# Optimization experiments

Hardware: AMD Instinct MI355X
Metric: run time of the kernel (lower is better)

## Reference

```python
import jax, jax.numpy as jnp
import numpy as np

NUM_HEADS = 16
DIM = 1024
HEAD_DIM = DIM // NUM_HEADS
SCALE = HEAD_DIM ** -0.5


def setup_inputs() -> dict:
    key = jax.random.key(0)
    ks = jax.random.split(key, 6)
    b, n = 2, 1024
    x = jax.random.normal(ks[0], (b, n, DIM), dtype=jnp.float32)
    Wq = jax.random.normal(ks[1], (DIM, DIM), dtype=jnp.float32) * 0.02
    bq = jnp.zeros((DIM,), dtype=jnp.float32)
    Wkv = jax.random.normal(ks[2], (2 * DIM, DIM), dtype=jnp.float32) * 0.02
    bkv = jnp.zeros((2 * DIM,), dtype=jnp.float32)
    Wp = jax.random.normal(ks[3], (DIM, DIM), dtype=jnp.float32) * 0.02
    bp = jnp.zeros((DIM,), dtype=jnp.float32)
    return {"x": x, "Wq": Wq, "bq": bq, "Wkv": Wkv, "bkv": bkv, "Wp": Wp, "bp": bp}


def reference(x, Wq, bq, Wkv, bkv, Wp, bp):
    b, n, c = x.shape
    h, dh = NUM_HEADS, HEAD_DIM
    # self-attention: y = x
    q = (x @ Wq.T + bq).reshape(b, n, h, dh)              # bnhd
    kv = (x @ Wkv.T + bkv).reshape(b, n, 2, h, dh)
    k, v = kv[:, :, 0], kv[:, :, 1]                       # bmhd each
    attn = jnp.einsum('bnhd,bmhd->bnmh', q, k) * SCALE    # bnmh scores
    attn = jax.nn.softmax(attn, axis=2)                   # softmax over m
    out = jnp.einsum('bnmh,bmhd->bnhd', attn, v).reshape(b, n, c)
    out = out @ Wp.T + bp
    return (out, attn)
```

## Files before the change

kernel.cpp:

```cpp
#include <hip/hip_runtime.h>
#include <hip/hip_bf16.h>
#include <stdint.h>


#define NB   2
#define SEQ  1024
#define CDIM 1024
#define NH   16
#define HD   64
#define ROWS (NB*SEQ)
#define ATT_SCALE 0.125f

typedef __attribute__((ext_vector_type(8))) short bf16x8;
typedef __attribute__((ext_vector_type(4))) float f32x4;

#define MFMA16(a,b,c) __builtin_amdgcn_mfma_f32_16x16x32_bf16((a),(b),(c),0,0,0)

static __device__ __forceinline__ unsigned short f2bf(float f) {
  uint32_t x = __builtin_bit_cast(uint32_t, f);
  return (unsigned short)((x + 0x7fffu + ((x >> 16) & 1u)) >> 16);
}
static __device__ __forceinline__ float bf2f(unsigned short u) {
  uint32_t x = ((uint32_t)u) << 16;
  return __builtin_bit_cast(float, x);
}

static __device__ __forceinline__ void gl_lds16(const unsigned short* g,
                                                unsigned short* l) {
  __builtin_amdgcn_global_load_lds(
      (const __attribute__((address_space(1))) unsigned int*)g,
      (__attribute__((address_space(3))) unsigned int*)l,
      16, 0, 0);
}

__global__ __launch_bounds__(256) void k_convert(
    const float* __restrict__ x, const float* __restrict__ Wq,
    const float* __restrict__ Wkv, const float* __restrict__ Wp,
    unsigned short* __restrict__ Xhi, unsigned short* __restrict__ Xlo,
    unsigned short* __restrict__ Whi, unsigned short* __restrict__ Wlo)
{
  const int NX = ROWS * CDIM;
  const int NW = 4096 * CDIM;
  int i = blockIdx.x * 256 + threadIdx.x;
  if (i < NX) {
    float f = x[i];
    unsigned short h = f2bf(f);
    Xhi[i] = h; Xlo[i] = f2bf(f - bf2f(h));
  } else if (i < NX + NW) {
    int w = i - NX;
    int j = w >> 10, c = w & 1023;
    float f = (j < 1024) ? Wq[(size_t)j*1024 + c]
            : (j < 3072) ? Wkv[(size_t)(j-1024)*1024 + c]
                         : Wp[(size_t)(j-3072)*1024 + c];
    unsigned short h = f2bf(f);
    Whi[w] = h; Wlo[w] = f2bf(f - bf2f(h));
  }
}

struct EpiQKV {
  const float* bq; const float* bkv;
  unsigned short *Qhi, *Qlo, *Khi, *Klo, *Vthi, *Vtlo;
  __device__ __forceinline__ void operator()(int m, int n, float v) const {
    if (n < 1024) {
      v = (v + bq[n]) * ATT_SCALE;
      unsigned short h = f2bf(v);
      size_t o = (size_t)m*1024 + n;
      Qhi[o] = h; Qlo[o] = f2bf(v - bf2f(h));
    } else if (n < 2048) {
      v += bkv[n - 1024];
      size_t o = (size_t)m*1024 + (n - 1024);
      unsigned short h = f2bf(v);
      Khi[o] = h; Klo[o] = f2bf(v - bf2f(h));
    } else {
      v += bkv[n - 1024];
      int c = n - 2048;
      int hh = c >> 6, d = c & 63;
      int b = m >> 10, mm = m & 1023;
      size_t o = ((size_t)((b*NH + hh)*HD + d))*SEQ + mm;
      unsigned short h = f2bf(v);
      Vthi[o] = h; Vtlo[o] = f2bf(v - bf2f(h));
    }
  }
};
struct EpiOut {
  const float* bp; float* out;
  __device__ __forceinline__ void operator()(int m, int n, float v) const {
    out[(size_t)m*1024 + n] = v + bp[n];
  }
};

template <int BM, int BN, class Epi>
__device__ __forceinline__ void gemm_core(
    const unsigned short* __restrict__ Ahi, const unsigned short* __restrict__ Alo, int lda,
    const unsigned short* __restrict__ Bhi, const unsigned short* __restrict__ Blo, int ldb,
    int K, const Epi& epi)
{
  constexpr int FM = BM/32, FN = BN/32;
  constexpr int CA = BM/16, CB = BN/16;
  constexpr int TOT = 2*(CA+CB);
  __shared__ unsigned short sAh[BM*32], sAl[BM*32], sBh[BN*32], sBl[BN*32];
  const int tid  = threadIdx.x;
  const int lane = tid & 63, wave = tid >> 6;
  const int wm = wave & 1, wn = wave >> 1;
  const int bn = blockIdx.x * BN, bm = blockIdx.y * BM;
  const int r = lane & 15, q = lane >> 4;
  const int crow = lane >> 2, ccol = (lane & 3) * 8;

  f32x4 acc[FM][FN];
  #pragma unroll
  for (int i = 0; i < FM; i++)
    #pragma unroll
    for (int j = 0; j < FN; j++) {
      acc[i][j][0]=0.f; acc[i][j][1]=0.f; acc[i][j][2]=0.f; acc[i][j][3]=0.f;
    }

  for (int k0 = 0; k0 < K; k0 += 32) {
    #pragma unroll
    for (int t = 0; t < TOT/4; t++) {
      int c = wave + t*4;
      const unsigned short* gb; unsigned short* sb; int rr, grow, ld;
      if (c < CA)            { gb=Ahi; sb=sAh; rr=c;         grow=bm; ld=lda; }
      else if (c < 2*CA)     { gb=Alo; sb=sAl; rr=c-CA;      grow=bm; ld=lda; }
      else if (c < 2*CA+CB)  { gb=Bhi; sb=sBh; rr=c-2*CA;    grow=bn; ld=ldb; }
      else                   { gb=Blo; sb=sBl; rr=c-2*CA-CB; grow=bn; ld=ldb; }
      int row = rr*16 + crow;
      gl_lds16(gb + (size_t)(grow + row)*ld + k0 + ccol, sb + rr*512);
    }
    __syncthreads();
    bf16x8 ah[FM], al[FM], bh[FN], bl[FN];
    #pragma unroll
    for (int i = 0; i < FM; i++) {
      int oa = (wm*(BM/2) + i*16 + r)*32 + q*8;
      ah[i] = *(const bf16x8*)(sAh + oa);
      al[i] = *(const bf16x8*)(sAl + oa);
    }
    #pragma unroll
    for (int j = 0; j < FN; j++) {
      int ob = (wn*(BN/2) + j*16 + r)*32 + q*8;
      bh[j] = *(const bf16x8*)(sBh + ob);
      bl[j] = *(const bf16x8*)(sBl + ob);
    }
    #pragma unroll
    for (int i = 0; i < FM; i++)
      #pragma unroll
      for (int j = 0; j < FN; j++) {
        acc[i][j] = MFMA16(ah[i], bh[j], acc[i][j]);
        acc[i][j] = MFMA16(ah[i], bl[j], acc[i][j]);
        acc[i][j] = MFMA16(al[i], bh[j], acc[i][j]);
      }
    __syncthreads();
  }
  #pragma unroll
  for (int i = 0; i < FM; i++)
    #pragma unroll
    for (int j = 0; j < FN; j++)
      #pragma unroll
      for (int t = 0; t < 4; t++)
        epi(bm + wm*(BM/2) + i*16 + q*4 + t, bn + wn*(BN/2) + j*16 + r, acc[i][j][t]);
}

__global__ __launch_bounds__(256) void k_gemm_qkv(
    const unsigned short* Xhi, const unsigned short* Xlo,
    const unsigned short* Whi, const unsigned short* Wlo,
    const float* bq, const float* bkv,
    unsigned short* Qhi, unsigned short* Qlo,
    unsigned short* Khi, unsigned short* Klo,
    unsigned short* Vthi, unsigned short* Vtlo)
{
  EpiQKV e{bq, bkv, Qhi, Qlo, Khi, Klo, Vthi, Vtlo};
  gemm_core<128,128>(Xhi, Xlo, CDIM, Whi, Wlo, CDIM, CDIM, e);
}

__global__ __launch_bounds__(256) void k_gemm_out(
    const unsigned short* OAhi, const unsigned short* OAlo,
    const unsigned short* Wphi, const unsigned short* Wplo,
    const float* bp, float* out)
{
  EpiOut e{bp, out};
  gemm_core<64,64>(OAhi, OAlo, CDIM, Wphi, Wplo, CDIM, CDIM, e);
}

__global__ __launch_bounds__(512, 4) void k_logits_softmax(
    const unsigned short* __restrict__ Qhi, const unsigned short* __restrict__ Qlo,
    const unsigned short* __restrict__ Khi, const unsigned short* __restrict__ Klo,
    unsigned short* __restrict__ P)
{
  const int nt = blockIdx.x, h = blockIdx.y, b = blockIdx.z;
  const int n0 = nt*32;
  const int col0 = h*HD;
  __shared__ unsigned short sQ[2*32*64];
  __shared__ unsigned short sK[2][2*128*64];
  __shared__ float redm[8][32], reds[8][32];
  __shared__ float gm_s[32], sc_s[32];
  const int tid = threadIdx.x, lane = tid & 63, wave = tid >> 6;
  const int r = lane & 15, q = lane >> 4;
  const int drow = lane >> 3, dseg = (lane & 7) ^ drow;
  const int sw = r & 7;
  const size_t qrow0 = (size_t)b*SEQ + n0;
  const size_t krow0 = (size_t)b*SEQ;

  auto stageK = [&](int c, int buf) {
    unsigned short* dst = sK[buf];
    #pragma unroll
    for (int u = 0; u < 4; u++) {
      int cc = wave*4 + u;
      int p = cc >> 4, t = cc & 15;
      const unsigned short* g = p ? Klo : Khi;
      gl_lds16(g + (krow0 + (size_t)c*128 + t*8 + drow)*CDIM + col0 + dseg*8,
               dst + p*8192 + t*512);
    }
  };

  {
    int p = wave >> 2, t = wave & 3;
    const unsigned short* g = p ? Qlo : Qhi;
    gl_lds16(g + (qrow0 + t*8 + drow)*CDIM + col0 + dseg*8,
             sQ + p*2048 + t*512);
    stageK(0, 0);
  }
  __syncthreads();

  bf16x8 qh[2][2], ql[2][2];
  #pragma unroll
  for (int nf = 0; nf < 2; nf++)
    #pragma unroll
    for (int ks = 0; ks < 2; ks++) {
      int phys = (nf*16 + r)*64 + (((ks*4 + q) ^ sw))*8;
      qh[nf][ks] = *(const bf16x8*)(sQ + phys);
      ql[nf][ks] = *(const bf16x8*)(sQ + 2048 + phys);
    }

  const int mb = wave*16;

  float mx[2] = {-1e30f, -1e30f}, sm[2] = {0.f, 0.f};
  for (int c = 0; c < 8; c++) {
    if (c < 7) stageK(c+1, (c+1)&1);
    const unsigned short* cur = sK[c&1];
    bf16x8 kh[2], kl[2];
    #pragma unroll
    for (int ks = 0; ks < 2; ks++) {
      int phys = (mb + r)*64 + (((ks*4 + q) ^ sw))*8;
      kh[ks] = *(const bf16x8*)(cur + phys);
      kl[ks] = *(const bf16x8*)(cur + 8192 + phys);
    }
    #pragma unroll
    for (int nf = 0; nf < 2; nf++) {
      f32x4 acc; acc[0]=0.f; acc[1]=0.f; acc[2]=0.f; acc[3]=0.f;
      #pragma unroll
      for (int ks = 0; ks < 2; ks++) {
        acc = MFMA16(kh[ks], qh[nf][ks], acc);
        acc = MFMA16(kl[ks], qh[nf][ks], acc);
        acc = MFMA16(kh[ks], ql[nf][ks], acc);
      }
      float vmax = fmaxf(fmaxf(acc[0], acc[1]), fmaxf(acc[2], acc[3]));
      float mnew = fmaxf(mx[nf], vmax);
      sm[nf] = sm[nf]*__expf(mx[nf]-mnew)
             + __expf(acc[0]-mnew) + __expf(acc[1]-mnew)
             + __expf(acc[2]-mnew) + __expf(acc[3]-mnew);
      mx[nf] = mnew;
    }
    __syncthreads();
  }

  #pragma unroll
  for (int nf = 0; nf < 2; nf++) {
    #pragma unroll
    for (int off = 16; off <= 32; off <<= 1) {
      float mo = __shfl_xor(mx[nf], off);
      float so = __shfl_xor(sm[nf], off);
      float mn = fmaxf(mx[nf], mo);
      sm[nf] = sm[nf]*__expf(mx[nf]-mn) + so*__expf(mo-mn);
      mx[nf] = mn;
    }
  }
  if (q < 2) { redm[wave][q*16 + r] = mx[q]; reds[wave][q*16 + r] = sm[q]; }
  stageK(0, 0);
  __syncthreads();
  if (tid < 32) {
    float m2 = redm[0][tid], s2 = reds[0][tid];
    #pragma unroll
    for (int w2 = 1; w2 < 8; w2++) {
      float mo = redm[w2][tid], so = reds[w2][tid];
      float mn = fmaxf(m2, mo);
      s2 = s2*__expf(m2-mn) + so*__expf(mo-mn);
      m2 = mn;
    }
    gm_s[tid] = m2; sc_s[tid] = 65535.0f / s2;
  }
  __syncthreads();
  const float gm[2] = {gm_s[r], gm_s[16 + r]};
  const float sc[2] = {sc_s[r], sc_s[16 + r]};

  const size_t pbase = ((size_t)(b*NH + h)*SEQ + n0)*SEQ;
  for (int c = 0; c < 8; c++) {
    if (c < 7) stageK(c+1, (c+1)&1);
    const unsigned short* cur = sK[c&1];
    bf16x8 kh[2], kl[2];
    #pragma unroll
    for (int ks = 0; ks < 2; ks++) {
      int phys = (mb + r)*64 + (((ks*4 + q) ^ sw))*8;
      kh[ks] = *(const bf16x8*)(cur + phys);
      kl[ks] = *(const bf16x8*)(cur + 8192 + phys);
    }
    #pragma unroll
    for (int nf = 0; nf < 2; nf++) {
      f32x4 acc; acc[0]=0.f; acc[1]=0.f; acc[2]=0.f; acc[3]=0.f;
      #pragma unroll
      for (int ks = 0; ks < 2; ks++) {
        acc = MFMA16(kh[ks], qh[nf][ks], acc);
        acc = MFMA16(kl[ks], qh[nf][ks], acc);
        acc = MFMA16(kh[ks], ql[nf][ks], acc);
      }
      unsigned int u0 = (unsigned)(__expf(acc[0]-gm[nf])*sc[nf] + 0.5f)
                      | ((unsigned)(__expf(acc[1]-gm[nf])*sc[nf] + 0.5f) << 16);
      unsigned int u1 = (unsigned)(__expf(acc[2]-gm[nf])*sc[nf] + 0.5f)
                      | ((unsigned)(__expf(acc[3]-gm[nf])*sc[nf] + 0.5f) << 16);
      *(uint2*)(P + pbase + (size_t)(nf*16 + r)*SEQ + c*128 + mb + q*4) =
          make_uint2(u0, u1);
    }
    __syncthreads();
  }
}

__global__ __launch_bounds__(256) void k_attn_write(
    const unsigned short* __restrict__ P, float* __restrict__ attn)
{
  int T = blockIdx.x*256 + threadIdx.x;
  int b = T >> 20, rem = T & 1048575;
  int n = rem >> 10, m = rem & 1023;
  const size_t pb = ((size_t)(b*NH)*SEQ + n)*SEQ + m;
  float v[16];
  #pragma unroll
  for (int h = 0; h < 16; h++)
    v[h] = (float)P[pb + (size_t)h*SEQ*SEQ] * (1.0f/65535.0f);
  size_t ob = ((size_t)(b*SEQ + n)*SEQ + m)*16;
  #pragma unroll
  for (int g = 0; g < 4; g++)
    *(float4*)(attn + ob + g*4) = make_float4(v[g*4], v[g*4+1], v[g*4+2], v[g*4+3]);
}

__global__ __launch_bounds__(256) void k_pv(
    const unsigned short* __restrict__ P,
    const unsigned short* __restrict__ Vthi, const unsigned short* __restrict__ Vtlo,
    unsigned short* __restrict__ OAhi, unsigned short* __restrict__ OAlo)
{
  int nt = blockIdx.x, h = blockIdx.y, b = blockIdx.z;
  int n0 = nt * 64;
  __shared__ unsigned short sPa[64*32], sPb[64*32], sVh[64*32], sVl[64*32];
  const int tid = threadIdx.x, lane = tid & 63, wave = tid >> 6;
  const int wm = wave & 1, wn = wave >> 1;
  const int r = lane & 15, q = lane >> 4;
  const int crow = lane >> 2, ccol = (lane & 3) * 8;
  const size_t pbase = ((size_t)(b*NH + h))*SEQ*SEQ;
  const size_t vbase = ((size_t)(b*NH + h))*HD*SEQ;

  f32x4 acc[2][2];
  #pragma unroll
  for (int i = 0; i < 2; i++)
    #pragma unroll
    for (int j = 0; j < 2; j++) {
      acc[i][j][0]=0.f; acc[i][j][1]=0.f; acc[i][j][2]=0.f; acc[i][j][3]=0.f;
    }

  for (int k0 = 0; k0 < SEQ; k0 += 32) {
    #pragma unroll
    for (int t = 0; t < 2; t++) {
      int c = wave + t*4;
      const unsigned short* gb = (c < 4) ? Vthi : Vtlo;
      unsigned short* sb = (c < 4) ? (unsigned short*)sVh : (unsigned short*)sVl;
      int rr = c & 3;
      int row = rr*16 + crow;
      gl_lds16(gb + vbase + (size_t)row*SEQ + k0 + ccol, sb + rr*512);
    }
    {
      int row = tid >> 2, ch = (tid & 3) * 8;
      uint4 v = *(const uint4*)(P + pbase + (size_t)(n0 + row)*SEQ + k0 + ch);
      unsigned int wds[4] = {v.x, v.y, v.z, v.w};
      unsigned int pa[4], pb4[4];
      #pragma unroll
      for (int e = 0; e < 4; e++) {
        unsigned int lo16 = wds[e] & 0xFFFFu;
        unsigned int hi16 = wds[e] >> 16;
        unsigned int a0 = __builtin_bit_cast(uint32_t, (float)(lo16 & 0xFF00u)) >> 16;
        unsigned int b0 = __builtin_bit_cast(uint32_t, (float)(lo16 & 0x00FFu)) >> 16;
        unsigned int a1 = __builtin_bit_cast(uint32_t, (float)(hi16 & 0xFF00u)) >> 16;
        unsigned int b1 = __builtin_bit_cast(uint32_t, (float)(hi16 & 0x00FFu)) >> 16;
        pa[e]  = a0 | (a1 << 16);
        pb4[e] = b0 | (b1 << 16);
      }
      *(uint4*)(sPa + row*32 + ch) = make_uint4(pa[0],pa[1],pa[2],pa[3]);
      *(uint4*)(sPb + row*32 + ch) = make_uint4(pb4[0],pb4[1],pb4[2],pb4[3]);
    }
    __syncthreads();
    bf16x8 pa[2], pb2[2], vh[2], vl[2];
    #pragma unroll
    for (int i = 0; i < 2; i++) {
      int off = (wm*32 + i*16 + r)*32 + q*8;
      pa[i]  = *(const bf16x8*)(sPa + off);
      pb2[i] = *(const bf16x8*)(sPb + off);
    }
    #pragma unroll
    for (int j = 0; j < 2; j++) {
      int off = (wn*32 + j*16 + r)*32 + q*8;
      vh[j] = *(const bf16x8*)(sVh + off);
      vl[j] = *(const bf16x8*)(sVl + off);
    }
    #pragma unroll
    for (int i = 0; i < 2; i++)
      #pragma unroll
      for (int j = 0; j < 2; j++) {
        acc[i][j] = MFMA16(pa[i],  vh[j], acc[i][j]);
        acc[i][j] = MFMA16(pb2[i], vh[j], acc[i][j]);
        acc[i][j] = MFMA16(pa[i],  vl[j], acc[i][j]);
      }
    __syncthreads();
  }
  #pragma unroll
  for (int i = 0; i < 2; i++)
    #pragma unroll
    for (int t = 0; t < 4; t++) {
      int nn = n0 + wm*32 + i*16 + q*4 + t;
      #pragma unroll
      for (int j = 0; j < 2; j++) {
        int d = wn*32 + j*16 + r;
        float val = acc[i][j][t] * (1.0f/65535.0f);
        size_t o = (size_t)(b*SEQ + nn)*CDIM + h*HD + d;
        unsigned short hb = f2bf(val);
        OAhi[o] = hb; OAlo[o] = f2bf(val - bf2f(hb));
      }
    }
}

extern "C" void kernel_launch(void* const* d_in, const int* in_sizes, int n_in,
                              void* d_out, int out_size, void* d_ws, size_t ws_size,
                              hipStream_t stream)
{
  const float* x   = (const float*)d_in[0];
  const float* Wq  = (const float*)d_in[1];
  const float* bq  = (const float*)d_in[2];
  const float* Wkv = (const float*)d_in[3];
  const float* bkv = (const float*)d_in[4];
  const float* Wp  = (const float*)d_in[5];
  const float* bp  = (const float*)d_in[6];

  float* out  = (float*)d_out;
  float* attn = out + (size_t)ROWS*CDIM;

  char* w = (char*)d_ws;
  unsigned short* Xhi  = (unsigned short*)w; w += (size_t)ROWS*CDIM*2;
  unsigned short* Xlo  = (unsigned short*)w; w += (size_t)ROWS*CDIM*2;
  unsigned short* Whi  = (unsigned short*)w; w += (size_t)4096*CDIM*2;
  unsigned short* Wlo  = (unsigned short*)w; w += (size_t)4096*CDIM*2;
  unsigned short* Qhi  = (unsigned short*)w; w += (size_t)ROWS*CDIM*2;
  unsigned short* Qlo  = (unsigned short*)w; w += (size_t)ROWS*CDIM*2;
  unsigned short* Khi  = (unsigned short*)w; w += (size_t)ROWS*CDIM*2;
  unsigned short* Klo  = (unsigned short*)w; w += (size_t)ROWS*CDIM*2;
  unsigned short* Vthi = (unsigned short*)w; w += (size_t)NB*NH*HD*SEQ*2;
  unsigned short* Vtlo = (unsigned short*)w; w += (size_t)NB*NH*HD*SEQ*2;
  unsigned short* OAhi = (unsigned short*)w; w += (size_t)ROWS*CDIM*2;
  unsigned short* OAlo = (unsigned short*)w; w += (size_t)ROWS*CDIM*2;
  unsigned short* P    = (unsigned short*)w; w += (size_t)NB*NH*SEQ*SEQ*2;

  k_convert<<<dim3((ROWS*CDIM + 4096*CDIM)/256), 256, 0, stream>>>(
      x, Wq, Wkv, Wp, Xhi, Xlo, Whi, Wlo);

  k_gemm_qkv<<<dim3(3072/128, 2048/128), 256, 0, stream>>>(
      Xhi, Xlo, Whi, Wlo, bq, bkv, Qhi, Qlo, Khi, Klo, Vthi, Vtlo);

  k_logits_softmax<<<dim3(SEQ/32, NH, NB), 512, 0, stream>>>(
      Qhi, Qlo, Khi, Klo, P);

  k_pv<<<dim3(SEQ/64, NH, NB), 256, 0, stream>>>(P, Vthi, Vtlo, OAhi, OAlo);

  k_gemm_out<<<dim3(1024/64, 2048/64), 256, 0, stream>>>(
      OAhi, OAlo, Whi + (size_t)3072*CDIM, Wlo + (size_t)3072*CDIM, bp, out);

  k_attn_write<<<dim3((NB*SEQ*SEQ)/256), 256, 0, stream>>>(P, attn);
}
```

Baseline: 394.5 us.

## Single-pass softmax with per-chunk rescale factors; retile output projection GEMM

The logits kernel now computes QK^T only once. Each 128-column chunk is quantized against the running row max, and a per-chunk correction factor (exp(m_c - m_final)/sum) is stored in a small table. The PV and attn_write kernels apply these factors, PV by folding them into its accumulator every 128 columns. This removes the second QK^T pass and its K re-staging, at the cost of an extra sync per chunk and some precision loss when early chunks are quantized against a smaller max. Separately, the output GEMM moves to 128x64 tiles with 8 waves, which halves its grid.

```diff
diff --git a/kernel.cpp b/kernel.cpp
--- a/kernel.cpp
+++ b/kernel.cpp
@@ -89,19 +89,20 @@
   }
 };
 
-template <int BM, int BN, class Epi>
+template <int BM, int BN, int WM, int WN, class Epi>
 __device__ __forceinline__ void gemm_core(
     const unsigned short* __restrict__ Ahi, const unsigned short* __restrict__ Alo, int lda,
     const unsigned short* __restrict__ Bhi, const unsigned short* __restrict__ Blo, int ldb,
     int K, const Epi& epi)
 {
-  constexpr int FM = BM/32, FN = BN/32;
+  constexpr int WAVES = WM*WN;
+  constexpr int FM = BM/(WM*16), FN = BN/(WN*16);
   constexpr int CA = BM/16, CB = BN/16;
   constexpr int TOT = 2*(CA+CB);
   __shared__ unsigned short sAh[BM*32], sAl[BM*32], sBh[BN*32], sBl[BN*32];
   const int tid  = threadIdx.x;
   const int lane = tid & 63, wave = tid >> 6;
-  const int wm = wave & 1, wn = wave >> 1;
+  const int wm = wave % WM, wn = wave / WM;
   const int bn = blockIdx.x * BN, bm = blockIdx.y * BM;
   const int r = lane & 15, q = lane >> 4;
   const int crow = lane >> 2, ccol = (lane & 3) * 8;
@@ -116,8 +117,8 @@
 
   for (int k0 = 0; k0 < K; k0 += 32) {
     #pragma unroll
-    for (int t = 0; t < TOT/4; t++) {
-      int c = wave + t*4;
+    for (int t = 0; t < TOT/WAVES; t++) {
+      int c = wave + t*WAVES;
       const unsigned short* gb; unsigned short* sb; int rr, grow, ld;
       if (c < CA)            { gb=Ahi; sb=sAh; rr=c;         grow=bm; ld=lda; }
       else if (c < 2*CA)     { gb=Alo; sb=sAl; rr=c-CA;      grow=bm; ld=lda; }
@@ -130,13 +131,13 @@
     bf16x8 ah[FM], al[FM], bh[FN], bl[FN];
     #pragma unroll
     for (int i = 0; i < FM; i++) {
-      int oa = (wm*(BM/2) + i*16 + r)*32 + q*8;
+      int oa = (wm*(BM/WM) + i*16 + r)*32 + q*8;
       ah[i] = *(const bf16x8*)(sAh + oa);
       al[i] = *(const bf16x8*)(sAl + oa);
     }
     #pragma unroll
     for (int j = 0; j < FN; j++) {
-      int ob = (wn*(BN/2) + j*16 + r)*32 + q*8;
+      int ob = (wn*(BN/WN) + j*16 + r)*32 + q*8;
       bh[j] = *(const bf16x8*)(sBh + ob);
       bl[j] = *(const bf16x8*)(sBl + ob);
     }
@@ -156,7 +157,7 @@
     for (int j = 0; j < FN; j++)
       #pragma unroll
       for (int t = 0; t < 4; t++)
-        epi(bm + wm*(BM/2) + i*16 + q*4 + t, bn + wn*(BN/2) + j*16 + r, acc[i][j][t]);
+        epi(bm + wm*(BM/WM) + i*16 + q*4 + t, bn + wn*(BN/WN) + j*16 + r, acc[i][j][t]);
 }
 
 __global__ __launch_bounds__(256) void k_gemm_qkv(
@@ -168,30 +169,31 @@
     unsigned short* Vthi, unsigned short* Vtlo)
 {
   EpiQKV e{bq, bkv, Qhi, Qlo, Khi, Klo, Vthi, Vtlo};
-  gemm_core<128,128>(Xhi, Xlo, CDIM, Whi, Wlo, CDIM, CDIM, e);
-}
-
-__global__ __launch_bounds__(256) void k_gemm_out(
+  gemm_core<128,128,2,2>(Xhi, Xlo, CDIM, Whi, Wlo, CDIM, CDIM, e);
+}
+
+__global__ __launch_bounds__(512) void k_gemm_out(
     const unsigned short* OAhi, const unsigned short* OAlo,
     const unsigned short* Wphi, const unsigned short* Wplo,
     const float* bp, float* out)
 {
   EpiOut e{bp, out};
-  gemm_core<64,64>(OAhi, OAlo, CDIM, Wphi, Wplo, CDIM, CDIM, e);
+  gemm_core<128,64,4,2>(OAhi, OAlo, CDIM, Wphi, Wplo, CDIM, CDIM, e);
 }
 
 __global__ __launch_bounds__(512, 4) void k_logits_softmax(
     const unsigned short* __restrict__ Qhi, const unsigned short* __restrict__ Qlo,
     const unsigned short* __restrict__ Khi, const unsigned short* __restrict__ Klo,
-    unsigned short* __restrict__ P)
+    unsigned short* __restrict__ P, float* __restrict__ F)
 {
   const int nt = blockIdx.x, h = blockIdx.y, b = blockIdx.z;
   const int n0 = nt*32;
   const int col0 = h*HD;
   __shared__ unsigned short sQ[2*32*64];
   __shared__ unsigned short sK[2][2*128*64];
-  __shared__ float redm[8][32], reds[8][32];
-  __shared__ float gm_s[32], sc_s[32];
+  __shared__ float redm[2][8][32];
+  __shared__ float reds[8][32];
+  __shared__ float musd[32][8];
   const int tid = threadIdx.x, lane = tid & 63, wave = tid >> 6;
   const int r = lane & 15, q = lane >> 4;
   const int drow = lane >> 3, dseg = (lane & 7) ^ drow;
@@ -231,8 +233,9 @@
     }
 
   const int mb = wave*16;
-
-  float mx[2] = {-1e30f, -1e30f}, sm[2] = {0.f, 0.f};
+  float m_run[2] = {-1e30f, -1e30f}, s_run[2] = {0.f, 0.f};
+  const size_t pbase = ((size_t)(b*NH + h)*SEQ + n0)*SEQ;
+
   for (int c = 0; c < 8; c++) {
     if (c < 7) stageK(c+1, (c+1)&1);
     const unsigned short* cur = sK[c&1];
@@ -243,96 +246,82 @@
       kh[ks] = *(const bf16x8*)(cur + phys);
       kl[ks] = *(const bf16x8*)(cur + 8192 + phys);
     }
+    f32x4 acc[2];
     #pragma unroll
     for (int nf = 0; nf < 2; nf++) {
-      f32x4 acc; acc[0]=0.f; acc[1]=0.f; acc[2]=0.f; acc[3]=0.f;
+      acc[nf][0]=0.f; acc[nf][1]=0.f; acc[nf][2]=0.f; acc[nf][3]=0.f;
       #pragma unroll
       for (int ks = 0; ks < 2; ks++) {
-        acc = MFMA16(kh[ks], qh[nf][ks], acc);
-        acc = MFMA16(kl[ks], qh[nf][ks], acc);
-        acc = MFMA16(kh[ks], ql[nf][ks], acc);
+        acc[nf] = MFMA16(kh[ks], qh[nf][ks], acc[nf]);
+        acc[nf] = MFMA16(kl[ks], qh[nf][ks], acc[nf]);
+        acc[nf] = MFMA16(kh[ks], ql[nf][ks], acc[nf]);
       }
-      float vmax = fmaxf(fmaxf(acc[0], acc[1]), fmaxf(acc[2], acc[3]));
-      float mnew = fmaxf(mx[nf], vmax);
-      sm[nf] = sm[nf]*__expf(mx[nf]-mnew)
-             + __expf(acc[0]-mnew) + __expf(acc[1]-mnew)
-             + __expf(acc[2]-mnew) + __expf(acc[3]-mnew);
-      mx[nf] = mnew;
-    }
+    }
+    float wmax[2];
+    #pragma unroll
+    for (int nf = 0; nf < 2; nf++) {
+      float v = fmaxf(fmaxf(acc[nf][0], acc[nf][1]), fmaxf(acc[nf][2], acc[nf][3]));
+      v = fmaxf(v, __shfl_xor(v, 16));
+      v = fmaxf(v, __shfl_xor(v, 32));
+      wmax[nf] = v;
+    }
+    if (q == 0) { redm[c&1][wave][r] = wmax[0]; redm[c&1][wave][16+r] = wmax[1]; }
     __syncthreads();
+    #pragma unroll
+    for (int nf = 0; nf < 2; nf++) {
+      int row = nf*16 + r;
+      float mc = redm[c&1][0][row];
+      #pragma unroll
+      for (int w2 = 1; w2 < 8; w2++) mc = fmaxf(mc, redm[c&1][w2][row]);
+      float mnew = fmaxf(m_run[nf], mc);
+      unsigned s0 = (unsigned)(__expf(acc[nf][0]-mnew)*65535.f + 0.5f);
+      unsigned s1 = (unsigned)(__expf(acc[nf][1]-mnew)*65535.f + 0.5f);
+      unsigned s2 = (unsigned)(__expf(acc[nf][2]-mnew)*65535.f + 0.5f);
+      unsigned s3 = (unsigned)(__expf(acc[nf][3]-mnew)*65535.f + 0.5f);
+      *(uint2*)(P + pbase + (size_t)row*SEQ + c*128 + mb + q*4) =
+          make_uint2(s0 | (s1 << 16), s2 | (s3 << 16));
+      s_run[nf] = s_run[nf]*__expf(m_run[nf]-mnew) + (float)(s0+s1+s2+s3);
+      m_run[nf] = mnew;
+      if (wave == 0 && q == 0) musd[row][c] = mnew;
+    }
   }
 
   #pragma unroll
   for (int nf = 0; nf < 2; nf++) {
-    #pragma unroll
-    for (int off = 16; off <= 32; off <<= 1) {
-      float mo = __shfl_xor(mx[nf], off);
-      float so = __shfl_xor(sm[nf], off);
-      float mn = fmaxf(mx[nf], mo);
-      sm[nf] = sm[nf]*__expf(mx[nf]-mn) + so*__expf(mo-mn);
-      mx[nf] = mn;
-    }
-  }
-  if (q < 2) { redm[wave][q*16 + r] = mx[q]; reds[wave][q*16 + r] = sm[q]; }
-  stageK(0, 0);
+    float s = s_run[nf];
+    s += __shfl_xor(s, 16);
+    s += __shfl_xor(s, 32);
+    if (q == 0) reds[wave][nf*16 + r] = s;
+  }
   __syncthreads();
   if (tid < 32) {
-    float m2 = redm[0][tid], s2 = reds[0][tid];
-    #pragma unroll
-    for (int w2 = 1; w2 < 8; w2++) {
-      float mo = redm[w2][tid], so = reds[w2][tid];
-      float mn = fmaxf(m2, mo);
-      s2 = s2*__expf(m2-mn) + so*__expf(mo-mn);
-      m2 = mn;
-    }
-    gm_s[tid] = m2; sc_s[tid] = 65535.0f / s2;
-  }
-  __syncthreads();
-  const float gm[2] = {gm_s[r], gm_s[16 + r]};
-  const float sc[2] = {sc_s[r], sc_s[16 + r]};
-
-  const size_t pbase = ((size_t)(b*NH + h)*SEQ + n0)*SEQ;
-  for (int c = 0; c < 8; c++) {
-    if (c < 7) stageK(c+1, (c+1)&1);
-    const unsigned short* cur = sK[c&1];
-    bf16x8 kh[2], kl[2];
-    #pragma unroll
-    for (int ks = 0; ks < 2; ks++) {
-      int phys = (mb + r)*64 + (((ks*4 + q) ^ sw))*8;
-      kh[ks] = *(const bf16x8*)(cur + phys);
-      kl[ks] = *(const bf16x8*)(cur + 8192 + phys);
-    }
-    #pragma unroll
-    for (int nf = 0; nf < 2; nf++) {
-      f32x4 acc; acc[0]=0.f; acc[1]=0.f; acc[2]=0.f; acc[3]=0.f;
-      #pragma unroll
-      for (int ks = 0; ks < 2; ks++) {
-        acc = MFMA16(kh[ks], qh[nf][ks], acc);
-        acc = MFMA16(kl[ks], qh[nf][ks], acc);
-        acc = MFMA16(kh[ks], ql[nf][ks], acc);
-      }
-      unsigned int u0 = (unsigned)(__expf(acc[0]-gm[nf])*sc[nf] + 0.5f)
-                      | ((unsigned)(__expf(acc[1]-gm[nf])*sc[nf] + 0.5f) << 16);
-      unsigned int u1 = (unsigned)(__expf(acc[2]-gm[nf])*sc[nf] + 0.5f)
-                      | ((unsigned)(__expf(acc[3]-gm[nf])*sc[nf] + 0.5f) << 16);
-      *(uint2*)(P + pbase + (size_t)(nf*16 + r)*SEQ + c*128 + mb + q*4) =
-          make_uint2(u0, u1);
-    }
-    __syncthreads();
+    int row = tid;
+    float S = 0.f;
+    #pragma unroll
+    for (int w2 = 0; w2 < 8; w2++) S += reds[w2][row];
+    float mfin = musd[row][7];
+    float inv = 1.0f / S;
+    size_t fb = ((size_t)(b*NH + h)*SEQ + n0 + row)*8;
+    #pragma unroll
+    for (int c = 0; c < 8; c++)
+      F[fb + c] = __expf(musd[row][c] - mfin) * inv;
   }
 }
 
 __global__ __launch_bounds__(256) void k_attn_write(
-    const unsigned short* __restrict__ P, float* __restrict__ attn)
+    const unsigned short* __restrict__ P, const float* __restrict__ F,
+    float* __restrict__ attn)
 {
   int T = blockIdx.x*256 + threadIdx.x;
   int b = T >> 20, rem = T & 1048575;
   int n = rem >> 10, m = rem & 1023;
+  int c = m >> 7;
   const size_t pb = ((size_t)(b*NH)*SEQ + n)*SEQ + m;
+  const size_t fb = ((size_t)(b*NH)*SEQ + n)*8 + c;
   float v[16];
   #pragma unroll
   for (int h = 0; h < 16; h++)
-    v[h] = (float)P[pb + (size_t)h*SEQ*SEQ] * (1.0f/65535.0f);
+    v[h] = (float)P[pb + (size_t)h*SEQ*SEQ] * F[fb + (size_t)h*SEQ*8];
   size_t ob = ((size_t)(b*SEQ + n)*SEQ + m)*16;
   #pragma unroll
   for (int g = 0; g < 4; g++)
@@ -340,7 +329,7 @@
 }
 
 __global__ __launch_bounds__(256) void k_pv(
-    const unsigned short* __restrict__ P,
+    const unsigned short* __restrict__ P, const float* __restrict__ F,
     const unsigned short* __restrict__ Vthi, const unsigned short* __restrict__ Vtlo,
     unsigned short* __restrict__ OAhi, unsigned short* __restrict__ OAlo)
 {
@@ -353,13 +342,15 @@
   const int crow = lane >> 2, ccol = (lane & 3) * 8;
   const size_t pbase = ((size_t)(b*NH + h))*SEQ*SEQ;
   const size_t vbase = ((size_t)(b*NH + h))*HD*SEQ;
-
-  f32x4 acc[2][2];
+  const size_t fbase = ((size_t)(b*NH + h))*SEQ*8;
+
+  f32x4 acc[2][2], accF[2][2];
   #pragma unroll
   for (int i = 0; i < 2; i++)
     #pragma unroll
     for (int j = 0; j < 2; j++) {
       acc[i][j][0]=0.f; acc[i][j][1]=0.f; acc[i][j][2]=0.f; acc[i][j][3]=0.f;
+      accF[i][j][0]=0.f; accF[i][j][1]=0.f; accF[i][j][2]=0.f; accF[i][j][3]=0.f;
     }
 
   for (int k0 = 0; k0 < SEQ; k0 += 32) {
@@ -413,6 +404,21 @@
         acc[i][j] = MFMA16(pb2[i], vh[j], acc[i][j]);
         acc[i][j] = MFMA16(pa[i],  vl[j], acc[i][j]);
       }
+    if ((k0 & 127) == 96) {
+      int c = k0 >> 7;
+      #pragma unroll
+      for (int i = 0; i < 2; i++)
+        #pragma unroll
+        for (int t = 0; t < 4; t++) {
+          int nn = n0 + wm*32 + i*16 + q*4 + t;
+          float Fv = F[fbase + (size_t)nn*8 + c];
+          #pragma unroll
+          for (int j = 0; j < 2; j++) {
+            accF[i][j][t] += acc[i][j][t] * Fv;
+            acc[i][j][t] = 0.f;
+          }
+        }
+    }
     __syncthreads();
   }
   #pragma unroll
@@ -423,7 +429,7 @@
       #pragma unroll
       for (int j = 0; j < 2; j++) {
         int d = wn*32 + j*16 + r;
-        float val = acc[i][j][t] * (1.0f/65535.0f);
+        float val = accF[i][j][t];
         size_t o = (size_t)(b*SEQ + nn)*CDIM + h*HD + d;
         unsigned short hb = f2bf(val);
         OAhi[o] = hb; OAlo[o] = f2bf(val - bf2f(hb));
@@ -460,6 +466,7 @@
   unsigned short* OAhi = (unsigned short*)w; w += (size_t)ROWS*CDIM*2;
   unsigned short* OAlo = (unsigned short*)w; w += (size_t)ROWS*CDIM*2;
   unsigned short* P    = (unsigned short*)w; w += (size_t)NB*NH*SEQ*SEQ*2;
+  float*          Ftab = (float*)w;          w += (size_t)NB*NH*SEQ*8*4;
 
   k_convert<<<dim3((ROWS*CDIM + 4096*CDIM)/256), 256, 0, stream>>>(
       x, Wq, Wkv, Wp, Xhi, Xlo, Whi, Wlo);
@@ -468,12 +475,12 @@
       Xhi, Xlo, Whi, Wlo, bq, bkv, Qhi, Qlo, Khi, Klo, Vthi, Vtlo);
 
   k_logits_softmax<<<dim3(SEQ/32, NH, NB), 512, 0, stream>>>(
-      Qhi, Qlo, Khi, Klo, P);
-
-  k_pv<<<dim3(SEQ/64, NH, NB), 256, 0, stream>>>(P, Vthi, Vtlo, OAhi, OAlo);
-
-  k_gemm_out<<<dim3(1024/64, 2048/64), 256, 0, stream>>>(
+      Qhi, Qlo, Khi, Klo, P, Ftab);
+
+  k_pv<<<dim3(SEQ/64, NH, NB), 256, 0, stream>>>(P, Ftab, Vthi, Vtlo, OAhi, OAlo);
+
+  k_gemm_out<<<dim3(1024/64, 2048/128), 512, 0, stream>>>(
       OAhi, OAlo, Whi + (size_t)3072*CDIM, Wlo + (size_t)3072*CDIM, bp, out);
 
-  k_attn_write<<<dim3((NB*SEQ*SEQ)/256), 256, 0, stream>>>(P, attn);
-}
+  k_attn_write<<<dim3((NB*SEQ*SEQ)/256), 256, 0, stream>>>(P, Ftab, attn);
+}
```

Result: faster. 385.4 us (-2.3%).
